# Kernel tuning notes

Measured on AMD Instinct MI355X. Metric: run time of the kernel, lower is better.

Reference implementation:

```python
import jax, jax.numpy as jnp
import numpy as np

D = 1280      # emb_dim
H = 4         # n_heads
DH = D // H
FF = 256      # dim_feedforward / hidden_dim
NL = 2        # n_layers
B = 64        # number of graphs
N = 32768     # total tokens
L = 640       # max padded length (>= max graph size w.h.p.)
EPS = 1e-5


def setup_inputs() -> dict:
    key = jax.random.key(0)
    ks = jax.random.split(key, 24)
    s = 0.02
    x = jax.random.normal(ks[0], (N, D), jnp.float32)
    batch = jnp.sort(jax.random.randint(ks[1], (N,), 0, B))
    p = {
        "x": x, "batch": batch,
        # stacked per-layer transformer params (torch Linear convention: y = x @ W.T + b)
        "Wqkv": jax.random.normal(ks[2], (NL, 3 * D, D), jnp.float32) * s,
        "bqkv": jnp.zeros((NL, 3 * D), jnp.float32),
        "Wo":   jax.random.normal(ks[3], (NL, D, D), jnp.float32) * s,
        "bo":   jnp.zeros((NL, D), jnp.float32),
        "ln1w": jnp.ones((NL, D), jnp.float32),
        "ln1b": jnp.zeros((NL, D), jnp.float32),
        "W1":   jax.random.normal(ks[4], (NL, FF, D), jnp.float32) * s,
        "b1":   jnp.zeros((NL, FF), jnp.float32),
        "W2":   jax.random.normal(ks[5], (NL, D, FF), jnp.float32) * s,
        "b2":   jnp.zeros((NL, D), jnp.float32),
        "ln2w": jnp.ones((NL, D), jnp.float32),
        "ln2b": jnp.zeros((NL, D), jnp.float32),
        # final MLP: Linear(D,FF) -> ReLU -> Linear(FF,D)
        "Wm1": jax.random.normal(ks[6], (FF, D), jnp.float32) * s,
        "bm1": jnp.zeros((FF,), jnp.float32),
        "Wm2": jax.random.normal(ks[7], (D, FF), jnp.float32) * s,
        "bm2": jnp.zeros((D,), jnp.float32),
    }
    return p


def _ln(x, w, b):
    mu = jnp.mean(x, axis=-1, keepdims=True)
    var = jnp.var(x, axis=-1, keepdims=True)
    return (x - mu) * jax.lax.rsqrt(var + EPS) * w + b


def reference(x, batch, Wqkv, bqkv, Wo, bo, ln1w, ln1b, W1, b1, W2, b2,
              ln2w, ln2b, Wm1, bm1, Wm2, bm2):
    # --- graph_to_transformer_input: scatter ragged tokens into [B, L, D] ---
    counts = jax.ops.segment_sum(jnp.ones_like(batch), batch, num_segments=B)
    offsets = jnp.concatenate([jnp.zeros((1,), counts.dtype), jnp.cumsum(counts)[:-1]])
    pos = jnp.arange(N) - offsets[batch]                 # position within each graph
    padded = jnp.zeros((B, L, D), x.dtype).at[batch, pos].set(x)
    pad_mask = jnp.arange(L)[None, :] >= counts[:, None]  # True = padding key

    h = padded
    scale = 1.0 / np.sqrt(DH)
    for l in range(NL):  # post-norm TransformerEncoderLayer, relu, dropout=eval
        qkv = h @ Wqkv[l].T + bqkv[l]
        q, k, v = jnp.split(qkv, 3, axis=-1)
        sh = lambda t: t.reshape(B, L, H, DH).transpose(0, 2, 1, 3)  # [B,H,L,DH]
        q, k, v = sh(q), sh(k), sh(v)
        scores = jnp.einsum('bhqd,bhkd->bhqk', q, k) * scale
        scores = jnp.where(pad_mask[:, None, None, :], -1e9, scores)
        attn = jax.nn.softmax(scores, axis=-1)
        o = jnp.einsum('bhqk,bhkd->bhqd', attn, v).transpose(0, 2, 1, 3).reshape(B, L, D)
        o = o @ Wo[l].T + bo[l]
        h = _ln(h + o, ln1w[l], ln1b[l])
        ff = jax.nn.relu(h @ W1[l].T + b1[l]) @ W2[l].T + b2[l]
        h = _ln(h + ff, ln2w[l], ln2b[l])

    forces = jax.nn.relu(h @ Wm1.T + bm1) @ Wm2.T + bm2   # [B, L, D]
    return forces[batch, pos]                              # gather valid tokens -> [N, D]
```

## Files before the change

kernel.cpp:

```cpp
#include <hip/hip_runtime.h>

typedef unsigned short u16;
typedef __attribute__((ext_vector_type(8))) short bf16x8;
typedef __attribute__((ext_vector_type(4))) float f32x4;

#define N_TOK 32768
#define DIM   1280
#define NH    4
#define DH    320
#define FFD   256
#define NLAYER 2
#define NB    64
#define TD    3840
#define KVD   2560

#define GLD16(gp, lp) __builtin_amdgcn_global_load_lds( \
    (const __attribute__((address_space(1))) unsigned int*)(const void*)(gp), \
    (__attribute__((address_space(3))) unsigned int*)(void*)(lp), 16, 0, 0)

__device__ __forceinline__ float b2f(u16 v) {
    union { unsigned u; float f; } c; c.u = ((unsigned)v) << 16; return c.f;
}
__device__ __forceinline__ u16 f2b(float f) {
    union { float f; unsigned u; } c; c.f = f;
    unsigned r = c.u + 0x7fffu + ((c.u >> 16) & 1u);
    return (u16)(r >> 16);
}

__global__ __launch_bounds__(256) void k_f32_to_bf16(
    const float* __restrict__ in, u16* __restrict__ out, long n)
{
    long i = ((long)blockIdx.x * 256 + threadIdx.x) * 4;
    if (i >= n) return;
    float4 v = *(const float4*)&in[i];
    ushort4 o; o.x = f2b(v.x); o.y = f2b(v.y); o.z = f2b(v.z); o.w = f2b(v.w);
    *(ushort4*)&out[i] = o;
}

__global__ void k_offsets(const int* __restrict__ batch, int* __restrict__ offs) {
    int b = threadIdx.x;
    if (b > NB) return;
    int lo = 0, hi = N_TOK;
    while (lo < hi) {
        int mid = (lo + hi) >> 1;
        if (batch[mid] < b) lo = mid + 1; else hi = mid;
    }
    offs[b] = lo;
}

__global__ __launch_bounds__(256) void k_gemm_mfma(
    const u16* __restrict__ A, int lda,
    const u16* __restrict__ W,
    const float* __restrict__ bias,
    void* __restrict__ Cv, int ldc,
    int K, int relu, int store_f32)
{
    __shared__ u16 Asm[128 * 64];
    __shared__ u16 Bsm[128 * 64];
    const int t    = threadIdx.x;
    const int lane = t & 63;
    const int w    = t >> 6;
    const int wr   = w >> 1, wc = w & 1;
    const long mBase = (long)blockIdx.y * 128;
    const long nBase = (long)blockIdx.x * 128;
    const int srow = lane >> 3;
    const int scol = (lane & 7) * 8;

    f32x4 acc[4][4];
    #pragma unroll
    for (int m = 0; m < 4; ++m)
        #pragma unroll
        for (int n = 0; n < 4; ++n) acc[m][n] = (f32x4){0.f, 0.f, 0.f, 0.f};

    for (int k0 = 0; k0 < K; k0 += 64) {
        __syncthreads();
        #pragma unroll
        for (int i = 0; i < 4; ++i) {
            const int c = w * 4 + i;
            const u16* ga = &A[(mBase + c * 8 + srow) * (long)lda + k0 + scol];
            const u16* gb = &W[(nBase + c * 8 + srow) * (long)K   + k0 + scol];
            GLD16(ga, &Asm[c * 512]);
            GLD16(gb, &Bsm[c * 512]);
        }
        __syncthreads();
        #pragma unroll
        for (int kk = 0; kk < 2; ++kk) {
            const int kc = kk * 32 + (lane >> 4) * 8;
            bf16x8 af[4], bfr[4];
            #pragma unroll
            for (int m = 0; m < 4; ++m)
                af[m] = *(const bf16x8*)&Asm[(wr * 64 + m * 16 + (lane & 15)) * 64 + kc];
            #pragma unroll
            for (int n = 0; n < 4; ++n)
                bfr[n] = *(const bf16x8*)&Bsm[(wc * 64 + n * 16 + (lane & 15)) * 64 + kc];
            #pragma unroll
            for (int m = 0; m < 4; ++m)
                #pragma unroll
                for (int n = 0; n < 4; ++n)
                    acc[m][n] = __builtin_amdgcn_mfma_f32_16x16x32_bf16(
                        af[m], bfr[n], acc[m][n], 0, 0, 0);
        }
    }

    const int ccol  = lane & 15;
    const int crow0 = (lane >> 4) * 4;
    #pragma unroll
    for (int m = 0; m < 4; ++m) {
        #pragma unroll
        for (int n = 0; n < 4; ++n) {
            const long col = nBase + wc * 64 + n * 16 + ccol;
            const float bv = bias[col];
            #pragma unroll
            for (int r = 0; r < 4; ++r) {
                const long row = mBase + wr * 64 + m * 16 + crow0 + r;
                float v = acc[m][n][r] + bv;
                if (relu) v = fmaxf(v, 0.f);
                if (store_f32) ((float*)Cv)[row * (long)ldc + col] = v;
                else           ((u16*)Cv)[row * (long)ldc + col] = f2b(v);
            }
        }
    }
}

__global__ __launch_bounds__(256) void k_ln_residual(
    const u16* __restrict__ a, const u16* __restrict__ delta,
    const float* __restrict__ w, const float* __restrict__ bb,
    u16* __restrict__ out)
{
    const long row = blockIdx.x;
    const int t = threadIdx.x;
    float v[5];
    float s = 0.f, s2 = 0.f;
    #pragma unroll
    for (int k = 0; k < 5; ++k) {
        int c = t + (k << 8);
        float xv = b2f(a[row * DIM + c]) + b2f(delta[row * DIM + c]);
        v[k] = xv; s += xv; s2 += xv * xv;
    }
    #pragma unroll
    for (int off = 32; off > 0; off >>= 1) {
        s  += __shfl_down(s, off);
        s2 += __shfl_down(s2, off);
    }
    __shared__ float red[8];
    __shared__ float stat[2];
    const int wid = t >> 6;
    if ((t & 63) == 0) { red[wid] = s; red[wid + 4] = s2; }
    __syncthreads();
    if (t == 0) {
        float S  = red[0] + red[1] + red[2] + red[3];
        float S2 = red[4] + red[5] + red[6] + red[7];
        float mu  = S * (1.f / DIM);
        float var = S2 * (1.f / DIM) - mu * mu;
        stat[0] = mu;
        stat[1] = rsqrtf(fmaxf(var, 0.f) + 1e-5f);
    }
    __syncthreads();
    float mu = stat[0], inv = stat[1];
    #pragma unroll
    for (int k = 0; k < 5; ++k) {
        int c = t + (k << 8);
        out[row * DIM + c] = f2b((v[k] - mu) * inv * w[c] + bb[c]);
    }
}

__global__ __launch_bounds__(256) void k_attn_mfma(
    u16* __restrict__ q, const u16* __restrict__ kv, const int* __restrict__ offs)
{
    __shared__ u16  Ks[32 * 328];
    __shared__ u16  Vt[320 * 36];
    __shared__ float Ssm[32 * 32];
    __shared__ u16  Plds[32 * 40];
    __shared__ float mL[32], lL[32], aL[32];

    const int qt = blockIdx.x;
    const int hh = blockIdx.y;
    const int b  = blockIdx.z;
    const int gstart = offs[b];
    const int n = offs[b + 1] - gstart;
    if (qt * 32 >= n) return;
    const int nq = min(32, n - qt * 32);
    const int t    = threadIdx.x;
    const int lane = t & 63;
    const int w    = t >> 6;
    const int qr   = w >> 1, kr = w & 1;
    const int l15  = lane & 15;
    const int l4   = lane >> 4;
    const float scale = 0.05590169943749474f;

    if (t < 32) { mL[t] = -1e30f; lL[t] = 0.f; }

    bf16x8 qf[10];
    {
        int qrl = qt * 32 + qr * 16 + l15;
        if (qrl >= n) qrl = n - 1;
        const u16* gq = &q[(long)(gstart + qrl) * DIM + hh * DH + l4 * 8];
        #pragma unroll
        for (int c = 0; c < 10; ++c)
            qf[c] = *(const bf16x8*)&gq[c * 32];
    }

    f32x4 oacc[2][5];
    #pragma unroll
    for (int a = 0; a < 2; ++a)
        #pragma unroll
        for (int f = 0; f < 5; ++f) oacc[a][f] = (f32x4){0.f, 0.f, 0.f, 0.f};

    __syncthreads();

    for (int kb = 0; kb < n; kb += 32) {
        const int nk = min(32, n - kb);
        __syncthreads();

        {
            const int pos = t >> 3;
            const int fb  = (t & 7) * 40;
            int gp = kb + pos; if (gp >= n) gp = n - 1;
            const u16* gk = &kv[(long)(gstart + gp) * KVD + hh * DH + fb];
            uint4 c0 = *(const uint4*)(gk + 0);
            uint4 c1 = *(const uint4*)(gk + 8);
            uint4 c2 = *(const uint4*)(gk + 16);
            uint4 c3 = *(const uint4*)(gk + 24);
            uint4 c4 = *(const uint4*)(gk + 32);
            u16* dst = &Ks[pos * 328 + fb];
            *(uint4*)(dst + 0)  = c0;
            *(uint4*)(dst + 8)  = c1;
            *(uint4*)(dst + 16) = c2;
            *(uint4*)(dst + 24) = c3;
            *(uint4*)(dst + 32) = c4;
        }
        {
            const int pp = t & 15;
            const int fb = (t >> 4) * 20;
            int p0 = kb + 2 * pp, p1 = p0 + 1;
            if (p0 >= n) p0 = n - 1;
            if (p1 >= n) p1 = n - 1;
            const u16* g0 = &kv[(long)(gstart + p0) * KVD + DIM + hh * DH + fb];
            const u16* g1 = &kv[(long)(gstart + p1) * KVD + DIM + hh * DH + fb];
            u16 va[20], vb[20];
            #pragma unroll
            for (int i = 0; i < 5; ++i) {
                *(uint2*)&va[i * 4] = *(const uint2*)(g0 + i * 4);
                *(uint2*)&vb[i * 4] = *(const uint2*)(g1 + i * 4);
            }
            #pragma unroll
            for (int f = 0; f < 20; ++f) {
                unsigned pk = (unsigned)va[f] | ((unsigned)vb[f] << 16);
                *(unsigned*)&Vt[(fb + f) * 36 + 2 * pp] = pk;
            }
        }
        __syncthreads();

        {
            f32x4 sacc = (f32x4){0.f, 0.f, 0.f, 0.f};
            #pragma unroll
            for (int c = 0; c < 10; ++c) {
                bf16x8 kf = *(const bf16x8*)&Ks[(kr * 16 + l15) * 328 + c * 32 + l4 * 8];
                sacc = __builtin_amdgcn_mfma_f32_16x16x32_bf16(qf[c], kf, sacc, 0, 0, 0);
            }
            const int col = kr * 16 + l15;
            const int srow0 = qr * 16 + l4 * 4;
            const bool masked = (col >= nk);
            #pragma unroll
            for (int r = 0; r < 4; ++r)
                Ssm[(srow0 + r) * 32 + col] = masked ? -1e30f : sacc[r] * scale;
        }
        __syncthreads();

        {
            const int r  = t >> 3;
            const int cg = (t & 7) * 4;
            float4 s4 = *(const float4*)&Ssm[r * 32 + cg];
            float mx = fmaxf(fmaxf(s4.x, s4.y), fmaxf(s4.z, s4.w));
            mx = fmaxf(mx, __shfl_xor(mx, 1));
            mx = fmaxf(mx, __shfl_xor(mx, 2));
            mx = fmaxf(mx, __shfl_xor(mx, 4));
            const float mo = mL[r];
            const float mn = fmaxf(mo, mx);
            float p0 = __expf(s4.x - mn), p1 = __expf(s4.y - mn);
            float p2 = __expf(s4.z - mn), p3 = __expf(s4.w - mn);
            union { u16 h[4]; uint2 u; } pw;
            pw.h[0] = f2b(p0); pw.h[1] = f2b(p1); pw.h[2] = f2b(p2); pw.h[3] = f2b(p3);
            *(uint2*)&Plds[r * 40 + cg] = pw.u;
            float rs = p0 + p1 + p2 + p3;
            rs += __shfl_xor(rs, 1);
            rs += __shfl_xor(rs, 2);
            rs += __shfl_xor(rs, 4);
            if ((t & 7) == 0) {
                const float al = __expf(mo - mn);
                aL[r] = al;
                lL[r] = lL[r] * al + rs;
                mL[r] = mn;
            }
        }
        __syncthreads();

        {
            float al[2][4];
            #pragma unroll
            for (int a = 0; a < 2; ++a)
                #pragma unroll
                for (int r = 0; r < 4; ++r)
                    al[a][r] = aL[a * 16 + l4 * 4 + r];
            #pragma unroll
            for (int a = 0; a < 2; ++a)
                #pragma unroll
                for (int f = 0; f < 5; ++f)
                    #pragma unroll
                    for (int r = 0; r < 4; ++r)
                        oacc[a][f][r] *= al[a][r];
            #pragma unroll
            for (int a = 0; a < 2; ++a) {
                bf16x8 pf = *(const bf16x8*)&Plds[(a * 16 + l15) * 40 + l4 * 8];
                #pragma unroll
                for (int f = 0; f < 5; ++f) {
                    const int fe = w * 80 + f * 16 + l15;
                    union { bf16x8 v; uint2 u[2]; } uv;
                    uv.u[0] = *(const uint2*)&Vt[fe * 36 + l4 * 8];
                    uv.u[1] = *(const uint2*)&Vt[fe * 36 + l4 * 8 + 4];
                    oacc[a][f] = __builtin_amdgcn_mfma_f32_16x16x32_bf16(
                        pf, uv.v, oacc[a][f], 0, 0, 0);
                }
            }
        }
    }

    float invl[2][4];
    #pragma unroll
    for (int a = 0; a < 2; ++a)
        #pragma unroll
        for (int r = 0; r < 4; ++r)
            invl[a][r] = 1.f / lL[a * 16 + l4 * 4 + r];
    #pragma unroll
    for (int a = 0; a < 2; ++a) {
        #pragma unroll
        for (int f = 0; f < 5; ++f) {
            #pragma unroll
            for (int r = 0; r < 4; ++r) {
                const int lrow = a * 16 + l4 * 4 + r;
                if (lrow < nq) {
                    const long grow = (long)(gstart + qt * 32 + lrow);
                    q[grow * DIM + hh * DH + w * 80 + f * 16 + l15] =
                        f2b(oacc[a][f][r] * invl[a][r]);
                }
            }
        }
    }
}

extern "C" void kernel_launch(void* const* d_in, const int* in_sizes, int n_in,
                              void* d_out, int out_size, void* d_ws, size_t ws_size,
                              hipStream_t stream) {
    const float* x     = (const float*)d_in[0];
    const int*   batch = (const int*)d_in[1];
    const float* Wqkv  = (const float*)d_in[2];
    const float* bqkv  = (const float*)d_in[3];
    const float* Wo    = (const float*)d_in[4];
    const float* bo    = (const float*)d_in[5];
    const float* ln1w  = (const float*)d_in[6];
    const float* ln1b  = (const float*)d_in[7];
    const float* W1    = (const float*)d_in[8];
    const float* b1    = (const float*)d_in[9];
    const float* W2    = (const float*)d_in[10];
    const float* b2    = (const float*)d_in[11];
    const float* ln2w  = (const float*)d_in[12];
    const float* ln2b  = (const float*)d_in[13];
    const float* Wm1   = (const float*)d_in[14];
    const float* bm1   = (const float*)d_in[15];
    const float* Wm2   = (const float*)d_in[16];
    const float* bm2   = (const float*)d_in[17];

    float* outF = (float*)d_out;
    u16*   qbuf = (u16*)d_out;

    char* ws   = (char*)d_ws;
    int*  offs = (int*)ws;
    u16*  h    = (u16*)(ws + 1024);
    u16*  kvb  = h + (size_t)N_TOK * DIM;
    u16*  tmp  = kvb;
    u16*  ff   = kvb + (size_t)N_TOK * DIM;
    u16*  wqkv_bf = kvb + (size_t)N_TOK * KVD;
    u16*  wo_bf   = wqkv_bf + (size_t)NLAYER * TD * DIM;
    u16*  w1_bf   = wo_bf   + (size_t)NLAYER * DIM * DIM;
    u16*  w2_bf   = w1_bf   + (size_t)NLAYER * FFD * DIM;
    u16*  wm1_bf  = w2_bf   + (size_t)NLAYER * DIM * FFD;
    u16*  wm2_bf  = wm1_bf  + (size_t)FFD * DIM;

    k_offsets<<<1, 128, 0, stream>>>(batch, offs);
    {
        long n = (long)N_TOK * DIM;
        k_f32_to_bf16<<<(int)(n / 1024), 256, 0, stream>>>(x, h, n);
        long nqkv = (long)NLAYER * TD * DIM;
        k_f32_to_bf16<<<(int)(nqkv / 1024), 256, 0, stream>>>(Wqkv, wqkv_bf, nqkv);
        long nwo = (long)NLAYER * DIM * DIM;
        k_f32_to_bf16<<<(int)(nwo / 1024), 256, 0, stream>>>(Wo, wo_bf, nwo);
        long nw1 = (long)NLAYER * FFD * DIM;
        k_f32_to_bf16<<<(int)(nw1 / 1024), 256, 0, stream>>>(W1, w1_bf, nw1);
        long nw2 = (long)NLAYER * DIM * FFD;
        k_f32_to_bf16<<<(int)(nw2 / 1024), 256, 0, stream>>>(W2, w2_bf, nw2);
        long nm = (long)FFD * DIM;
        k_f32_to_bf16<<<(int)(nm / 1024), 256, 0, stream>>>(Wm1, wm1_bf, nm);
        k_f32_to_bf16<<<(int)(nm / 1024), 256, 0, stream>>>(Wm2, wm2_bf, nm);
    }

    dim3 blk(256);
    for (int l = 0; l < NLAYER; ++l) {
        const u16*   Wl = wqkv_bf + (size_t)l * TD * DIM;
        const float* bl = bqkv + (size_t)l * TD;
        k_gemm_mfma<<<dim3(DIM / 128, N_TOK / 128), blk, 0, stream>>>(
            h, DIM, Wl, bl, qbuf, DIM, DIM, 0, 0);
        k_gemm_mfma<<<dim3(KVD / 128, N_TOK / 128), blk, 0, stream>>>(
            h, DIM, Wl + (size_t)DIM * DIM, bl + DIM, kvb, KVD, DIM, 0, 0);
        k_attn_mfma<<<dim3(20, NH, NB), blk, 0, stream>>>(qbuf, kvb, offs);
        k_gemm_mfma<<<dim3(DIM / 128, N_TOK / 128), blk, 0, stream>>>(
            qbuf, DIM, wo_bf + (size_t)l * DIM * DIM, bo + (size_t)l * DIM,
            tmp, DIM, DIM, 0, 0);
        k_ln_residual<<<N_TOK, blk, 0, stream>>>(
            h, tmp, ln1w + (size_t)l * DIM, ln1b + (size_t)l * DIM, h);
        k_gemm_mfma<<<dim3(FFD / 128, N_TOK / 128), blk, 0, stream>>>(
            h, DIM, w1_bf + (size_t)l * FFD * DIM, b1 + (size_t)l * FFD,
            ff, FFD, DIM, 1, 0);
        k_gemm_mfma<<<dim3(DIM / 128, N_TOK / 128), blk, 0, stream>>>(
            ff, FFD, w2_bf + (size_t)l * DIM * FFD, b2 + (size_t)l * DIM,
            tmp, DIM, FFD, 0, 0);
        k_ln_residual<<<N_TOK, blk, 0, stream>>>(
            h, tmp, ln2w + (size_t)l * DIM, ln2b + (size_t)l * DIM, h);
    }
    k_gemm_mfma<<<dim3(FFD / 128, N_TOK / 128), blk, 0, stream>>>(
        h, DIM, wm1_bf, bm1, ff, FFD, DIM, 1, 0);
    k_gemm_mfma<<<dim3(DIM / 128, N_TOK / 128), blk, 0, stream>>>(
        ff, FFD, wm2_bf, bm2, outF, DIM, FFD, 0, 1);
}
```

Baseline: 2.800 ms.

## Give each attention wave its own 16 query rows with register-resident online softmax

The attention block grows from 32 to 64 query rows, with each wave owning 16 rows and all 320 head dims. Each K/V tile staged in shared memory is therefore reused by twice as many queries, and the grid shrinks from 20 to 10 query tiles. Softmax max, sum and rescale now run in registers with lane shuffles instead of going through shared score, max and sum arrays, which removes two block-wide barriers per key tile. In exchange each thread holds 20 accumulator fragments, which raises register pressure and may lower occupancy.

```diff
diff --git a/kernel.cpp b/kernel.cpp
--- a/kernel.cpp
+++ b/kernel.cpp
@@ -167,32 +167,27 @@
 __global__ __launch_bounds__(256) void k_attn_mfma(
     u16* __restrict__ q, const u16* __restrict__ kv, const int* __restrict__ offs)
 {
-    __shared__ u16  Ks[32 * 328];
-    __shared__ u16  Vt[320 * 36];
-    __shared__ float Ssm[32 * 32];
-    __shared__ u16  Plds[32 * 40];
-    __shared__ float mL[32], lL[32], aL[32];
+    __shared__ u16 Ks[32 * 328];
+    __shared__ u16 Vt[320 * 36];
+    __shared__ u16 Plds[64 * 40];
 
     const int qt = blockIdx.x;
     const int hh = blockIdx.y;
     const int b  = blockIdx.z;
     const int gstart = offs[b];
     const int n = offs[b + 1] - gstart;
-    if (qt * 32 >= n) return;
-    const int nq = min(32, n - qt * 32);
+    if (qt * 64 >= n) return;
+    const int nq = min(64, n - qt * 64);
     const int t    = threadIdx.x;
     const int lane = t & 63;
     const int w    = t >> 6;
-    const int qr   = w >> 1, kr = w & 1;
     const int l15  = lane & 15;
     const int l4   = lane >> 4;
     const float scale = 0.05590169943749474f;
 
-    if (t < 32) { mL[t] = -1e30f; lL[t] = 0.f; }
-
     bf16x8 qf[10];
     {
-        int qrl = qt * 32 + qr * 16 + l15;
+        int qrl = qt * 64 + w * 16 + l15;
         if (qrl >= n) qrl = n - 1;
         const u16* gq = &q[(long)(gstart + qrl) * DIM + hh * DH + l4 * 8];
         #pragma unroll
@@ -200,13 +195,11 @@
             qf[c] = *(const bf16x8*)&gq[c * 32];
     }
 
-    f32x4 oacc[2][5];
-    #pragma unroll
-    for (int a = 0; a < 2; ++a)
-        #pragma unroll
-        for (int f = 0; f < 5; ++f) oacc[a][f] = (f32x4){0.f, 0.f, 0.f, 0.f};
-
-    __syncthreads();
+    f32x4 oacc[20];
+    #pragma unroll
+    for (int f = 0; f < 20; ++f) oacc[f] = (f32x4){0.f, 0.f, 0.f, 0.f};
+    float m_r[4] = {-1e30f, -1e30f, -1e30f, -1e30f};
+    float l_r[4] = {0.f, 0.f, 0.f, 0.f};
 
     for (int kb = 0; kb < n; kb += 32) {
         const int nk = min(32, n - kb);
@@ -251,98 +244,76 @@
         }
         __syncthreads();
 
-        {
-            f32x4 sacc = (f32x4){0.f, 0.f, 0.f, 0.f};
+        f32x4 sacc[2];
+        #pragma unroll
+        for (int kr = 0; kr < 2; ++kr) {
+            sacc[kr] = (f32x4){0.f, 0.f, 0.f, 0.f};
             #pragma unroll
             for (int c = 0; c < 10; ++c) {
                 bf16x8 kf = *(const bf16x8*)&Ks[(kr * 16 + l15) * 328 + c * 32 + l4 * 8];
-                sacc = __builtin_amdgcn_mfma_f32_16x16x32_bf16(qf[c], kf, sacc, 0, 0, 0);
+                sacc[kr] = __builtin_amdgcn_mfma_f32_16x16x32_bf16(qf[c], kf, sacc[kr], 0, 0, 0);
             }
-            const int col = kr * 16 + l15;
-            const int srow0 = qr * 16 + l4 * 4;
-            const bool masked = (col >= nk);
+        }
+        float sv[2][4];
+        #pragma unroll
+        for (int kr = 0; kr < 2; ++kr) {
+            const bool masked = (kr * 16 + l15) >= nk;
             #pragma unroll
             for (int r = 0; r < 4; ++r)
-                Ssm[(srow0 + r) * 32 + col] = masked ? -1e30f : sacc[r] * scale;
-        }
-        __syncthreads();
-
-        {
-            const int r  = t >> 3;
-            const int cg = (t & 7) * 4;
-            float4 s4 = *(const float4*)&Ssm[r * 32 + cg];
-            float mx = fmaxf(fmaxf(s4.x, s4.y), fmaxf(s4.z, s4.w));
+                sv[kr][r] = masked ? -1e30f : sacc[kr][r] * scale;
+        }
+        float al[4], pr[2][4], rs[4];
+        #pragma unroll
+        for (int r = 0; r < 4; ++r) {
+            float mx = fmaxf(sv[0][r], sv[1][r]);
             mx = fmaxf(mx, __shfl_xor(mx, 1));
             mx = fmaxf(mx, __shfl_xor(mx, 2));
             mx = fmaxf(mx, __shfl_xor(mx, 4));
-            const float mo = mL[r];
-            const float mn = fmaxf(mo, mx);
-            float p0 = __expf(s4.x - mn), p1 = __expf(s4.y - mn);
-            float p2 = __expf(s4.z - mn), p3 = __expf(s4.w - mn);
-            union { u16 h[4]; uint2 u; } pw;
-            pw.h[0] = f2b(p0); pw.h[1] = f2b(p1); pw.h[2] = f2b(p2); pw.h[3] = f2b(p3);
-            *(uint2*)&Plds[r * 40 + cg] = pw.u;
-            float rs = p0 + p1 + p2 + p3;
-            rs += __shfl_xor(rs, 1);
-            rs += __shfl_xor(rs, 2);
-            rs += __shfl_xor(rs, 4);
-            if ((t & 7) == 0) {
-                const float al = __expf(mo - mn);
-                aL[r] = al;
-                lL[r] = lL[r] * al + rs;
-                mL[r] = mn;
-            }
-        }
-        __syncthreads();
-
-        {
-            float al[2][4];
-            #pragma unroll
-            for (int a = 0; a < 2; ++a)
-                #pragma unroll
-                for (int r = 0; r < 4; ++r)
-                    al[a][r] = aL[a * 16 + l4 * 4 + r];
-            #pragma unroll
-            for (int a = 0; a < 2; ++a)
-                #pragma unroll
-                for (int f = 0; f < 5; ++f)
-                    #pragma unroll
-                    for (int r = 0; r < 4; ++r)
-                        oacc[a][f][r] *= al[a][r];
-            #pragma unroll
-            for (int a = 0; a < 2; ++a) {
-                bf16x8 pf = *(const bf16x8*)&Plds[(a * 16 + l15) * 40 + l4 * 8];
-                #pragma unroll
-                for (int f = 0; f < 5; ++f) {
-                    const int fe = w * 80 + f * 16 + l15;
-                    union { bf16x8 v; uint2 u[2]; } uv;
-                    uv.u[0] = *(const uint2*)&Vt[fe * 36 + l4 * 8];
-                    uv.u[1] = *(const uint2*)&Vt[fe * 36 + l4 * 8 + 4];
-                    oacc[a][f] = __builtin_amdgcn_mfma_f32_16x16x32_bf16(
-                        pf, uv.v, oacc[a][f], 0, 0, 0);
-                }
-            }
-        }
-    }
-
-    float invl[2][4];
-    #pragma unroll
-    for (int a = 0; a < 2; ++a)
-        #pragma unroll
-        for (int r = 0; r < 4; ++r)
-            invl[a][r] = 1.f / lL[a * 16 + l4 * 4 + r];
-    #pragma unroll
-    for (int a = 0; a < 2; ++a) {
-        #pragma unroll
-        for (int f = 0; f < 5; ++f) {
-            #pragma unroll
-            for (int r = 0; r < 4; ++r) {
-                const int lrow = a * 16 + l4 * 4 + r;
-                if (lrow < nq) {
-                    const long grow = (long)(gstart + qt * 32 + lrow);
-                    q[grow * DIM + hh * DH + w * 80 + f * 16 + l15] =
-                        f2b(oacc[a][f][r] * invl[a][r]);
-                }
+            mx = fmaxf(mx, __shfl_xor(mx, 8));
+            const float mn = fmaxf(m_r[r], mx);
+            al[r] = __expf(m_r[r] - mn);
+            m_r[r] = mn;
+            pr[0][r] = __expf(sv[0][r] - mn);
+            pr[1][r] = __expf(sv[1][r] - mn);
+            float s = pr[0][r] + pr[1][r];
+            s += __shfl_xor(s, 1);
+            s += __shfl_xor(s, 2);
+            s += __shfl_xor(s, 4);
+            s += __shfl_xor(s, 8);
+            rs[r] = s;
+            l_r[r] = l_r[r] * al[r] + rs[r];
+        }
+        #pragma unroll
+        for (int kr = 0; kr < 2; ++kr)
+            #pragma unroll
+            for (int r = 0; r < 4; ++r)
+                Plds[(w * 16 + l4 * 4 + r) * 40 + kr * 16 + l15] = f2b(pr[kr][r]);
+        #pragma unroll
+        for (int f = 0; f < 20; ++f)
+            #pragma unroll
+            for (int r = 0; r < 4; ++r)
+                oacc[f][r] *= al[r];
+        bf16x8 pf = *(const bf16x8*)&Plds[(w * 16 + l15) * 40 + l4 * 8];
+        #pragma unroll
+        for (int f = 0; f < 20; ++f) {
+            union { bf16x8 v; uint2 u[2]; } uv;
+            uv.u[0] = *(const uint2*)&Vt[(f * 16 + l15) * 36 + l4 * 8];
+            uv.u[1] = *(const uint2*)&Vt[(f * 16 + l15) * 36 + l4 * 8 + 4];
+            oacc[f] = __builtin_amdgcn_mfma_f32_16x16x32_bf16(pf, uv.v, oacc[f], 0, 0, 0);
+        }
+    }
+
+    float invl[4];
+    #pragma unroll
+    for (int r = 0; r < 4; ++r) invl[r] = 1.f / l_r[r];
+    #pragma unroll
+    for (int f = 0; f < 20; ++f) {
+        #pragma unroll
+        for (int r = 0; r < 4; ++r) {
+            const int lrow = w * 16 + l4 * 4 + r;
+            if (lrow < nq) {
+                const long grow = (long)(gstart + qt * 64 + lrow);
+                q[grow * DIM + hh * DH + f * 16 + l15] = f2b(oacc[f][r] * invl[r]);
             }
         }
     }
@@ -411,7 +382,7 @@
             h, DIM, Wl, bl, qbuf, DIM, DIM, 0, 0);
         k_gemm_mfma<<<dim3(KVD / 128, N_TOK / 128), blk, 0, stream>>>(
             h, DIM, Wl + (size_t)DIM * DIM, bl + DIM, kvb, KVD, DIM, 0, 0);
-        k_attn_mfma<<<dim3(20, NH, NB), blk, 0, stream>>>(qbuf, kvb, offs);
+        k_attn_mfma<<<dim3(10, NH, NB), blk, 0, stream>>>(qbuf, kvb, offs);
         k_gemm_mfma<<<dim3(DIM / 128, N_TOK / 128), blk, 0, stream>>>(
             qbuf, DIM, wo_bf + (size_t)l * DIM * DIM, bo + (size_t)l * DIM,
             tmp, DIM, DIM, 0, 0);
```

After: 3.204 ms. 1.14x slower.

## Alias K and V LDS buffers, defer V transpose, remap attention grid

Applied to the files above, without the earlier changes.

The attention kernel now shares one LDS buffer between the K tile and the transposed V tile, so shared memory per block shrinks and launch_bounds can ask for 4 blocks per CU. V is loaded into registers early and written to LDS after the QK scores are consumed, which overlaps the global load with the score MFMAs and softmax. The S scratch row stride is padded to 33 to reduce bank conflicts. The grid is flattened and remapped so blocks from 8 graphs interleave across the GPU, which aims to balance ragged work and improve L2 locality. The extra live registers and the tighter occupancy bound risk spills.

```diff
diff --git a/kernel.cpp b/kernel.cpp
--- a/kernel.cpp
+++ b/kernel.cpp
@@ -164,20 +164,24 @@
     }
 }
 
-__global__ __launch_bounds__(256) void k_attn_mfma(
+__global__ __launch_bounds__(256, 4) void k_attn_mfma(
     u16* __restrict__ q, const u16* __restrict__ kv, const int* __restrict__ offs)
 {
-    __shared__ u16  Ks[32 * 328];
-    __shared__ u16  Vt[320 * 36];
-    __shared__ float Ssm[32 * 32];
-    __shared__ u16  Plds[32 * 40];
+    __shared__ u16 KV[11520];
+    __shared__ float Ssm[32 * 33];
+    __shared__ u16 Plds[32 * 40];
     __shared__ float mL[32], lL[32], aL[32];
 
-    const int qt = blockIdx.x;
-    const int hh = blockIdx.y;
-    const int b  = blockIdx.z;
-    const int gstart = offs[b];
-    const int n = offs[b + 1] - gstart;
+    const int lin = blockIdx.x;
+    const int gLo = lin & 7;
+    const int j   = lin >> 3;
+    const int g   = (j / 80) * 8 + gLo;
+    const int rem = j % 80;
+    const int hh  = rem / 20;
+    const int qt  = rem % 20;
+
+    const int gstart = offs[g];
+    const int n = offs[g + 1] - gstart;
     if (qt * 32 >= n) return;
     const int nq = min(32, n - qt * 32);
     const int t    = threadIdx.x;
@@ -206,56 +210,50 @@
         #pragma unroll
         for (int f = 0; f < 5; ++f) oacc[a][f] = (f32x4){0.f, 0.f, 0.f, 0.f};
 
-    __syncthreads();
+    const int spos = t >> 3;
+    const int sfb  = (t & 7) * 40;
+    const int vpp  = t & 15;
+    const int vfb  = (t >> 4) * 20;
 
     for (int kb = 0; kb < n; kb += 32) {
         const int nk = min(32, n - kb);
         __syncthreads();
 
+        uint2 va4[5], vb4[5];
         {
-            const int pos = t >> 3;
-            const int fb  = (t & 7) * 40;
-            int gp = kb + pos; if (gp >= n) gp = n - 1;
-            const u16* gk = &kv[(long)(gstart + gp) * KVD + hh * DH + fb];
+            int p0 = kb + 2 * vpp, p1 = p0 + 1;
+            if (p0 >= n) p0 = n - 1;
+            if (p1 >= n) p1 = n - 1;
+            const u16* g0 = &kv[(long)(gstart + p0) * KVD + DIM + hh * DH + vfb];
+            const u16* g1 = &kv[(long)(gstart + p1) * KVD + DIM + hh * DH + vfb];
+            #pragma unroll
+            for (int i = 0; i < 5; ++i) {
+                va4[i] = *(const uint2*)(g0 + i * 4);
+                vb4[i] = *(const uint2*)(g1 + i * 4);
+            }
+        }
+        {
+            int gp = kb + spos; if (gp >= n) gp = n - 1;
+            const u16* gk = &kv[(long)(gstart + gp) * KVD + hh * DH + sfb];
             uint4 c0 = *(const uint4*)(gk + 0);
             uint4 c1 = *(const uint4*)(gk + 8);
             uint4 c2 = *(const uint4*)(gk + 16);
             uint4 c3 = *(const uint4*)(gk + 24);
             uint4 c4 = *(const uint4*)(gk + 32);
-            u16* dst = &Ks[pos * 328 + fb];
+            u16* dst = &KV[spos * 328 + sfb];
             *(uint4*)(dst + 0)  = c0;
             *(uint4*)(dst + 8)  = c1;
             *(uint4*)(dst + 16) = c2;
             *(uint4*)(dst + 24) = c3;
             *(uint4*)(dst + 32) = c4;
         }
-        {
-            const int pp = t & 15;
-            const int fb = (t >> 4) * 20;
-            int p0 = kb + 2 * pp, p1 = p0 + 1;
-            if (p0 >= n) p0 = n - 1;
-            if (p1 >= n) p1 = n - 1;
-            const u16* g0 = &kv[(long)(gstart + p0) * KVD + DIM + hh * DH + fb];
-            const u16* g1 = &kv[(long)(gstart + p1) * KVD + DIM + hh * DH + fb];
-            u16 va[20], vb[20];
-            #pragma unroll
-            for (int i = 0; i < 5; ++i) {
-                *(uint2*)&va[i * 4] = *(const uint2*)(g0 + i * 4);
-                *(uint2*)&vb[i * 4] = *(const uint2*)(g1 + i * 4);
-            }
-            #pragma unroll
-            for (int f = 0; f < 20; ++f) {
-                unsigned pk = (unsigned)va[f] | ((unsigned)vb[f] << 16);
-                *(unsigned*)&Vt[(fb + f) * 36 + 2 * pp] = pk;
-            }
-        }
         __syncthreads();
 
         {
             f32x4 sacc = (f32x4){0.f, 0.f, 0.f, 0.f};
             #pragma unroll
             for (int c = 0; c < 10; ++c) {
-                bf16x8 kf = *(const bf16x8*)&Ks[(kr * 16 + l15) * 328 + c * 32 + l4 * 8];
+                bf16x8 kf = *(const bf16x8*)&KV[(kr * 16 + l15) * 328 + c * 32 + l4 * 8];
                 sacc = __builtin_amdgcn_mfma_f32_16x16x32_bf16(qf[c], kf, sacc, 0, 0, 0);
             }
             const int col = kr * 16 + l15;
@@ -263,14 +261,14 @@
             const bool masked = (col >= nk);
             #pragma unroll
             for (int r = 0; r < 4; ++r)
-                Ssm[(srow0 + r) * 32 + col] = masked ? -1e30f : sacc[r] * scale;
+                Ssm[(srow0 + r) * 33 + col] = masked ? -1e30f : sacc[r] * scale;
         }
         __syncthreads();
 
         {
             const int r  = t >> 3;
             const int cg = (t & 7) * 4;
-            float4 s4 = *(const float4*)&Ssm[r * 32 + cg];
+            float4 s4 = *(const float4*)&Ssm[r * 33 + cg];
             float mx = fmaxf(fmaxf(s4.x, s4.y), fmaxf(s4.z, s4.w));
             mx = fmaxf(mx, __shfl_xor(mx, 1));
             mx = fmaxf(mx, __shfl_xor(mx, 2));
@@ -292,6 +290,16 @@
                 lL[r] = lL[r] * al + rs;
                 mL[r] = mn;
             }
+            #pragma unroll
+            for (int i = 0; i < 5; ++i) {
+                const unsigned a0 = va4[i].x, a1 = va4[i].y;
+                const unsigned b0 = vb4[i].x, b1 = vb4[i].y;
+                const int fb = vfb + i * 4;
+                *(unsigned*)&KV[(fb + 0) * 36 + 2 * vpp] = (a0 & 0xffffu) | (b0 << 16);
+                *(unsigned*)&KV[(fb + 1) * 36 + 2 * vpp] = (a0 >> 16) | (b0 & 0xffff0000u);
+                *(unsigned*)&KV[(fb + 2) * 36 + 2 * vpp] = (a1 & 0xffffu) | (b1 << 16);
+                *(unsigned*)&KV[(fb + 3) * 36 + 2 * vpp] = (a1 >> 16) | (b1 & 0xffff0000u);
+            }
         }
         __syncthreads();
 
@@ -316,8 +324,8 @@
                 for (int f = 0; f < 5; ++f) {
                     const int fe = w * 80 + f * 16 + l15;
                     union { bf16x8 v; uint2 u[2]; } uv;
-                    uv.u[0] = *(const uint2*)&Vt[fe * 36 + l4 * 8];
-                    uv.u[1] = *(const uint2*)&Vt[fe * 36 + l4 * 8 + 4];
+                    uv.u[0] = *(const uint2*)&KV[fe * 36 + l4 * 8];
+                    uv.u[1] = *(const uint2*)&KV[fe * 36 + l4 * 8 + 4];
                     oacc[a][f] = __builtin_amdgcn_mfma_f32_16x16x32_bf16(
                         pf, uv.v, oacc[a][f], 0, 0, 0);
                 }
@@ -411,7 +419,7 @@
             h, DIM, Wl, bl, qbuf, DIM, DIM, 0, 0);
         k_gemm_mfma<<<dim3(KVD / 128, N_TOK / 128), blk, 0, stream>>>(
             h, DIM, Wl + (size_t)DIM * DIM, bl + DIM, kvb, KVD, DIM, 0, 0);
-        k_attn_mfma<<<dim3(20, NH, NB), blk, 0, stream>>>(qbuf, kvb, offs);
+        k_attn_mfma<<<dim3(20 * NH * NB), blk, 0, stream>>>(qbuf, kvb, offs);
         k_gemm_mfma<<<dim3(DIM / 128, N_TOK / 128), blk, 0, stream>>>(
             qbuf, DIM, wo_bf + (size_t)l * DIM * DIM, bo + (size_t)l * DIM,
             tmp, DIM, DIM, 0, 0);
```

New measurement: 3.021 ms. 1.08x slower.
